# Performance work log

Hardware: AMD Instinct MI355X
Metric: run time of the kernel (lower is better)

The kernel has to match this reference:

```python
import jax, jax.numpy as jnp
import numpy as np

DIM = 512
HEADS = 8
DIM_HEAD = 64
DIM_INNER = HEADS * DIM_HEAD  # 512
SCALE = DIM_HEAD ** -0.5


def setup_inputs() -> dict:
    key = jax.random.key(0)
    k1, k2, k3 = jax.random.split(key, 3)
    x = jax.random.normal(k1, (8, 2048, DIM), dtype=jnp.float32)
    # Linear weights (no bias). Stored as [in, out] for x @ W.
    w_qkv = jax.random.normal(k2, (DIM, 3 * DIM_INNER), dtype=jnp.float32) * (DIM ** -0.5)
    w_out = jax.random.normal(k3, (DIM_INNER, DIM), dtype=jnp.float32) * (DIM_INNER ** -0.5)
    return {"x": x, "w_qkv": w_qkv, "w_out": w_out}


def reference(x, w_qkv, w_out):
    b, n, _ = x.shape
    qkv = x @ w_qkv  # [b, n, 3*h*d]
    qkv = qkv.reshape(b, n, 3, HEADS, DIM_HEAD)
    qkv = jnp.transpose(qkv, (2, 0, 3, 1, 4))  # [3, b, h, n, d]
    q, k, v = qkv[0], qkv[1], qkv[2]
    q = q * SCALE
    sim = jnp.einsum('bhid,bhjd->bhij', q, k)
    attn = jax.nn.softmax(sim, axis=-1)
    out = jnp.einsum('bhij,bhjd->bhid', attn, v)  # [b, h, n, d]
    out = jnp.transpose(out, (0, 2, 1, 3)).reshape(b, n, DIM_INNER)
    return out @ w_out
```

## Files before the change

kernel.cpp:

```cpp
#include <hip/hip_runtime.h>
#include <hip/hip_bf16.h>
#include <stdint.h>


#define NB 8
#define SEQ 2048
#define DIMM 512
#define HEADS 8
#define DHEAD 64
#define MTOT (NB * SEQ)

typedef __attribute__((ext_vector_type(8))) short bf16x8;
typedef __attribute__((ext_vector_type(4))) float f32x4;
typedef __attribute__((ext_vector_type(16))) float f32x16;
typedef __attribute__((ext_vector_type(4))) uint u32x4;

typedef __attribute__((address_space(1))) const void gconst_void;
typedef __attribute__((address_space(3))) void lds_void;

__device__ __forceinline__ ushort f2b(float f) {
  union { float f; uint32_t u; } c; c.f = f;
  return (ushort)((c.u + 0x7FFFu + ((c.u >> 16) & 1u)) >> 16);
}

__device__ __forceinline__ uint cvtpk(float lo, float hi) {
  uint r;
  asm("v_cvt_pk_bf16_f32 %0, %1, %2" : "=v"(r) : "v"(lo), "v"(hi));
  return r;
}
__device__ __forceinline__ void plswap(uint& a, uint& b) {
  asm("v_permlane32_swap_b32 %0, %1" : "+v"(a), "+v"(b));
}
__device__ __forceinline__ bf16x8 mk8(uint a, uint b, uint c, uint d) {
  u32x4 t = {a, b, c, d};
  return __builtin_bit_cast(bf16x8, t);
}

__global__ void cvt_bf16(const float* __restrict__ src, ushort* __restrict__ dst, int n8) {
  int i = blockIdx.x * blockDim.x + threadIdx.x;
  if (i >= n8) return;
  const float4* s = (const float4*)src;
  float4 a = s[2 * i], b = s[2 * i + 1];
  ushort o[8] = {f2b(a.x), f2b(a.y), f2b(a.z), f2b(a.w),
                 f2b(b.x), f2b(b.y), f2b(b.z), f2b(b.w)};
  *(uint4*)(dst + 8 * i) = *(const uint4*)o;
}

__global__ void cvt_transpose(const float* __restrict__ src, ushort* __restrict__ dst,
                              int R, int C) {
  __shared__ ushort tile[64][72];
  int nbc = C >> 6;
  int bc = blockIdx.x % nbc, br = blockIdx.x / nbc;
  int c0 = bc * 64, r0 = br * 64;
  #pragma unroll
  for (int p = 0; p < 16; ++p) {
    int e = p * 256 + threadIdx.x;
    int r = e >> 6, c = e & 63;
    tile[r][c] = f2b(src[(size_t)(r0 + r) * C + c0 + c]);
  }
  __syncthreads();
  #pragma unroll
  for (int p = 0; p < 16; ++p) {
    int e = p * 256 + threadIdx.x;
    int ct = e >> 6, rt = e & 63;
    dst[(size_t)(c0 + ct) * R + r0 + rt] = tile[rt][ct];
  }
}

__global__ __launch_bounds__(256) void gemm_qkv(
    const ushort* __restrict__ A, const ushort* __restrict__ Bt,
    ushort* __restrict__ qo, ushort* __restrict__ ko, ushort* __restrict__ vto) {
  __shared__ ushort As[128 * 64];
  __shared__ ushort Bs[128 * 64];
  const int tid = threadIdx.x;
  const int bid = blockIdx.x;
  const int sbid = (bid & 7) * 192 + (bid >> 3);
  const int bn = sbid % 12, bm = sbid / 12;
  const int wid = tid >> 6, lane = tid & 63;
  const int wm = (wid >> 1) * 64, wn = (wid & 1) * 64;
  const int lr = lane & 15, lk = (lane >> 4) * 8;
  const int fx = lr & 7;

  f32x4 acc[4][4] = {};
  const ushort* Ab = A + (size_t)(bm * 128) * DIMM;
  const ushort* Bb = Bt + (size_t)(bn * 128) * DIMM;

  const int srow = lane >> 3;
  const int sco = ((lane & 7) ^ srow) << 3;

  for (int kt = 0; kt < DIMM; kt += 64) {
    __syncthreads();
    #pragma unroll
    for (int j = 0; j < 4; ++j) {
      const int c = wid * 4 + j;
      const size_t ro = (size_t)(8 * c + srow) * DIMM + kt + sco;
      __builtin_amdgcn_global_load_lds((gconst_void*)(Ab + ro),
                                       (lds_void*)&As[c * 512], 16, 0, 0);
      __builtin_amdgcn_global_load_lds((gconst_void*)(Bb + ro),
                                       (lds_void*)&Bs[c * 512], 16, 0, 0);
    }
    asm volatile("s_waitcnt vmcnt(0)" ::: "memory");
    __syncthreads();

    #pragma unroll
    for (int kk = 0; kk < 64; kk += 32) {
      const int sb = (kk >> 3) + (lane >> 4);
      const int so = (sb ^ fx) << 3;
      bf16x8 af[4], bfr[4];
      #pragma unroll
      for (int i = 0; i < 4; ++i) af[i] = *(const bf16x8*)&As[(wm + i * 16 + lr) * 64 + so];
      #pragma unroll
      for (int j = 0; j < 4; ++j) bfr[j] = *(const bf16x8*)&Bs[(wn + j * 16 + lr) * 64 + so];
      #pragma unroll
      for (int i = 0; i < 4; ++i)
        #pragma unroll
        for (int j = 0; j < 4; ++j)
          acc[i][j] = __builtin_amdgcn_mfma_f32_16x16x32_bf16(af[i], bfr[j], acc[i][j], 0, 0, 0);
    }
  }

  const int rb = bm * 128 + wm + ((lane >> 4) << 2);
  const int cb = bn * 128 + wn + lr;
  const float QSCALE = 0.125f * 1.44269504f;
  #pragma unroll
  for (int i = 0; i < 4; ++i) {
    #pragma unroll
    for (int j = 0; j < 4; ++j) {
      int col = cb + j * 16;
      int t = col >> 9, h = (col >> 6) & 7, d = col & 63;
      f32x4 v = acc[i][j];
      #pragma unroll
      for (int e = 0; e < 4; ++e) {
        int row = rb + i * 16 + e;
        int b = row >> 11, n = row & 2047;
        float val = v[e];
        if (t == 0) {
          qo[(((size_t)b * HEADS + h) * SEQ + n) * DHEAD + d] = f2b(val * QSCALE);
        } else if (t == 1) {
          ko[(((size_t)b * HEADS + h) * SEQ + n) * DHEAD + d] = f2b(val);
        } else {
          vto[(((size_t)b * HEADS + h) * DHEAD + d) * SEQ + n] = f2b(val);
        }
      }
    }
  }
}

__global__ __launch_bounds__(256) void gemm_out(
    const ushort* __restrict__ A, const ushort* __restrict__ Bt, float* __restrict__ out) {
  __shared__ ushort As[128 * 64];
  __shared__ ushort Bs[128 * 64];
  const int tid = threadIdx.x;
  const int bid = blockIdx.x;
  const int sbid = (bid & 7) * 64 + (bid >> 3);
  const int bn = sbid % 4, bm = sbid / 4;
  const int wid = tid >> 6, lane = tid & 63;
  const int wm = (wid >> 1) * 64, wn = (wid & 1) * 64;
  const int lr = lane & 15, lk = (lane >> 4) * 8;
  const int fx = lr & 7;

  f32x4 acc[4][4] = {};
  const ushort* Ab = A + (size_t)(bm * 128) * DIMM;
  const ushort* Bb = Bt + (size_t)(bn * 128) * DIMM;

  const int srow = lane >> 3;
  const int sco = ((lane & 7) ^ srow) << 3;

  for (int kt = 0; kt < DIMM; kt += 64) {
    __syncthreads();
    #pragma unroll
    for (int j = 0; j < 4; ++j) {
      const int c = wid * 4 + j;
      const size_t ro = (size_t)(8 * c + srow) * DIMM + kt + sco;
      __builtin_amdgcn_global_load_lds((gconst_void*)(Ab + ro),
                                       (lds_void*)&As[c * 512], 16, 0, 0);
      __builtin_amdgcn_global_load_lds((gconst_void*)(Bb + ro),
                                       (lds_void*)&Bs[c * 512], 16, 0, 0);
    }
    asm volatile("s_waitcnt vmcnt(0)" ::: "memory");
    __syncthreads();

    #pragma unroll
    for (int kk = 0; kk < 64; kk += 32) {
      const int sb = (kk >> 3) + (lane >> 4);
      const int so = (sb ^ fx) << 3;
      bf16x8 af[4], bfr[4];
      #pragma unroll
      for (int i = 0; i < 4; ++i) af[i] = *(const bf16x8*)&As[(wm + i * 16 + lr) * 64 + so];
      #pragma unroll
      for (int j = 0; j < 4; ++j) bfr[j] = *(const bf16x8*)&Bs[(wn + j * 16 + lr) * 64 + so];
      #pragma unroll
      for (int i = 0; i < 4; ++i)
        #pragma unroll
        for (int j = 0; j < 4; ++j)
          acc[i][j] = __builtin_amdgcn_mfma_f32_16x16x32_bf16(af[i], bfr[j], acc[i][j], 0, 0, 0);
    }
  }

  const int rb = bm * 128 + wm + ((lane >> 4) << 2);
  const int cb = bn * 128 + wn + lr;
  #pragma unroll
  for (int i = 0; i < 4; ++i)
    #pragma unroll
    for (int j = 0; j < 4; ++j) {
      f32x4 v = acc[i][j];
      #pragma unroll
      for (int e = 0; e < 4; ++e)
        out[(size_t)(rb + i * 16 + e) * DIMM + cb + j * 16] = v[e];
    }
}

__global__ __launch_bounds__(256) void attn(
    const ushort* __restrict__ q, const ushort* __restrict__ k,
    const ushort* __restrict__ vt, ushort* __restrict__ ao) {
  __shared__ ushort Ks[64 * 64];
  __shared__ ushort Vs[64 * 64];

  const int tid = threadIdx.x;
  const int wid = tid >> 6, l = tid & 63;
  const int l31 = l & 31, hi = l >> 5;
  const int bh = blockIdx.x >> 4, qb = blockIdx.x & 15;
  const ushort* kb = k + (size_t)bh * SEQ * DHEAD;
  const ushort* vb = vt + (size_t)bh * DHEAD * SEQ;
  const int nq = qb * 128 + wid * 32 + l31;

  bf16x8 qf[4];
  const ushort* qrow = q + (size_t)bh * SEQ * DHEAD + (size_t)nq * DHEAD;
  #pragma unroll
  for (int ks = 0; ks < 4; ++ks)
    qf[ks] = *(const bf16x8*)(qrow + ks * 16 + hi * 8);

  f32x16 accO0 = {}, accO1 = {};
  float lrun = 0.f;

  const int sr = tid >> 3, sc = tid & 7;
  const int swz = (sc ^ (sr & 7)) << 3;
  uint4 k0 = *(const uint4*)(kb + (size_t)sr * DHEAD + sc * 8);
  uint4 k1 = *(const uint4*)(kb + (size_t)(sr + 32) * DHEAD + sc * 8);
  uint4 v0 = *(const uint4*)(vb + (size_t)sr * SEQ + sc * 8);
  uint4 v1 = *(const uint4*)(vb + (size_t)(sr + 32) * SEQ + sc * 8);

  const int fsx = (l31 & 7);

  for (int t = 0; t < SEQ / 64; ++t) {
    __syncthreads();
    *(uint4*)&Ks[sr * 64 + swz] = k0;
    *(uint4*)&Ks[(sr + 32) * 64 + swz] = k1;
    *(uint4*)&Vs[sr * 64 + swz] = v0;
    *(uint4*)&Vs[(sr + 32) * 64 + swz] = v1;
    __syncthreads();

    if (t + 1 < SEQ / 64) {
      int nt = (t + 1) * 64;
      k0 = *(const uint4*)(kb + (size_t)(nt + sr) * DHEAD + sc * 8);
      k1 = *(const uint4*)(kb + (size_t)(nt + sr + 32) * DHEAD + sc * 8);
      v0 = *(const uint4*)(vb + (size_t)sr * SEQ + nt + sc * 8);
      v1 = *(const uint4*)(vb + (size_t)(sr + 32) * SEQ + nt + sc * 8);
    }

    f32x16 s0 = {}, s1 = {};
    #pragma unroll
    for (int ks = 0; ks < 4; ++ks) {
      int g = (ks << 1) | hi;
      int so = (g ^ fsx) << 3;
      bf16x8 kf0 = *(const bf16x8*)&Ks[l31 * 64 + so];
      bf16x8 kf1 = *(const bf16x8*)&Ks[(32 + l31) * 64 + so];
      s0 = __builtin_amdgcn_mfma_f32_32x32x16_bf16(kf0, qf[ks], s0, 0, 0, 0);
      s1 = __builtin_amdgcn_mfma_f32_32x32x16_bf16(kf1, qf[ks], s1, 0, 0, 0);
    }

    float rs = 0.f;
    #pragma unroll
    for (int i = 0; i < 16; ++i) {
      s0[i] = __builtin_amdgcn_exp2f(s0[i]); rs += s0[i];
      s1[i] = __builtin_amdgcn_exp2f(s1[i]); rs += s1[i];
    }
    rs += __shfl_xor(rs, 32);
    lrun += rs;

    bf16x8 pf0, pf1, pf2, pf3;
    {
      uint a0 = cvtpk(s0[0], s0[1]),  a1 = cvtpk(s0[2], s0[3]);
      uint b0 = cvtpk(s0[4], s0[5]),  b1 = cvtpk(s0[6], s0[7]);
      plswap(a0, b0); plswap(a1, b1);
      pf0 = mk8(a0, a1, b0, b1);
      a0 = cvtpk(s0[8], s0[9]);   a1 = cvtpk(s0[10], s0[11]);
      b0 = cvtpk(s0[12], s0[13]); b1 = cvtpk(s0[14], s0[15]);
      plswap(a0, b0); plswap(a1, b1);
      pf1 = mk8(a0, a1, b0, b1);
      a0 = cvtpk(s1[0], s1[1]);   a1 = cvtpk(s1[2], s1[3]);
      b0 = cvtpk(s1[4], s1[5]);   b1 = cvtpk(s1[6], s1[7]);
      plswap(a0, b0); plswap(a1, b1);
      pf2 = mk8(a0, a1, b0, b1);
      a0 = cvtpk(s1[8], s1[9]);   a1 = cvtpk(s1[10], s1[11]);
      b0 = cvtpk(s1[12], s1[13]); b1 = cvtpk(s1[14], s1[15]);
      plswap(a0, b0); plswap(a1, b1);
      pf3 = mk8(a0, a1, b0, b1);
    }

    #pragma unroll
    for (int kk = 0; kk < 4; ++kk) {
      int g = (kk << 1) | hi;
      int so = (g ^ fsx) << 3;
      bf16x8 vf0 = *(const bf16x8*)&Vs[l31 * 64 + so];
      bf16x8 vf1 = *(const bf16x8*)&Vs[(32 + l31) * 64 + so];
      bf16x8 pk = (kk == 0) ? pf0 : (kk == 1) ? pf1 : (kk == 2) ? pf2 : pf3;
      accO0 = __builtin_amdgcn_mfma_f32_32x32x16_bf16(vf0, pk, accO0, 0, 0, 0);
      accO1 = __builtin_amdgcn_mfma_f32_32x32x16_bf16(vf1, pk, accO1, 0, 0, 0);
    }
  }

  const int b = bh >> 3, h = bh & 7;
  const float rl = 1.0f / lrun;
  ushort* aop = ao + ((size_t)b * SEQ + nq) * DIMM + h * DHEAD;
  #pragma unroll
  for (int gq = 0; gq < 4; ++gq) {
    {
      int d0 = 8 * gq + 4 * hi;
      uint u0 = (uint)f2b(accO0[4 * gq + 0] * rl) | ((uint)f2b(accO0[4 * gq + 1] * rl) << 16);
      uint u1 = (uint)f2b(accO0[4 * gq + 2] * rl) | ((uint)f2b(accO0[4 * gq + 3] * rl) << 16);
      *(uint2*)(aop + d0) = make_uint2(u0, u1);
    }
    {
      int d0 = 32 + 8 * gq + 4 * hi;
      uint u0 = (uint)f2b(accO1[4 * gq + 0] * rl) | ((uint)f2b(accO1[4 * gq + 1] * rl) << 16);
      uint u1 = (uint)f2b(accO1[4 * gq + 2] * rl) | ((uint)f2b(accO1[4 * gq + 3] * rl) << 16);
      *(uint2*)(aop + d0) = make_uint2(u0, u1);
    }
  }
}

extern "C" void kernel_launch(void* const* d_in, const int* in_sizes, int n_in,
                              void* d_out, int out_size, void* d_ws, size_t ws_size,
                              hipStream_t stream) {
  const float* x = (const float*)d_in[0];
  const float* wqkv = (const float*)d_in[1];
  const float* wout = (const float*)d_in[2];
  float* out = (float*)d_out;

  char* ws = (char*)d_ws;
  const size_t SZ = (size_t)MTOT * DIMM * 2;
  ushort* xb    = (ushort*)(ws);
  ushort* qw    = (ushort*)(ws + SZ);
  ushort* kw    = (ushort*)(ws + 2 * SZ);
  ushort* vtw   = (ushort*)(ws + 3 * SZ);
  ushort* aow   = (ushort*)(ws + 4 * SZ);
  ushort* wqkvT = (ushort*)(ws + 5 * SZ);
  ushort* woutT = (ushort*)(ws + 5 * SZ + (size_t)1536 * 512 * 2);

  hipLaunchKernelGGL(cvt_bf16, dim3(4096), dim3(256), 0, stream, x, xb, MTOT * DIMM / 8);
  hipLaunchKernelGGL(cvt_transpose, dim3(192), dim3(256), 0, stream, wqkv, wqkvT, 512, 1536);
  hipLaunchKernelGGL(cvt_transpose, dim3(64), dim3(256), 0, stream, wout, woutT, 512, 512);
  hipLaunchKernelGGL(gemm_qkv, dim3(128 * 12), dim3(256), 0, stream, xb, wqkvT, qw, kw, vtw);
  hipLaunchKernelGGL(attn, dim3(64 * 16), dim3(256), 0, stream, qw, kw, vtw, aow);
  hipLaunchKernelGGL(gemm_out, dim3(128 * 4), dim3(256), 0, stream, aow, woutT, out);
}
```

Measured before the change: 196.5 us.

## Load K/V MFMA fragments directly from global memory, dropping LDS staging

The attention kernel no longer stages K and V tiles through shared memory with register prefetch and two barriers per iteration. Each wave now reads its MFMA operand fragments straight from global memory (relying on L1/L2 for reuse across the four waves), and the launch bounds ask for 4 blocks per CU. This removes the LDS writes, the barriers and the swizzle arithmetic, but exposes global-load latency in the inner loop with no explicit prefetch and repeats each K/V load across waves.

```diff
diff --git a/kernel.cpp b/kernel.cpp
--- a/kernel.cpp
+++ b/kernel.cpp
@@ -210,12 +210,9 @@
     }
 }
 
-__global__ __launch_bounds__(256) void attn(
+__global__ __launch_bounds__(256, 4) void attn(
     const ushort* __restrict__ q, const ushort* __restrict__ k,
     const ushort* __restrict__ vt, ushort* __restrict__ ao) {
-  __shared__ ushort Ks[64 * 64];
-  __shared__ ushort Vs[64 * 64];
-
   const int tid = threadIdx.x;
   const int wid = tid >> 6, l = tid & 63;
   const int l31 = l & 31, hi = l >> 5;
@@ -233,38 +230,17 @@
   f32x16 accO0 = {}, accO1 = {};
   float lrun = 0.f;
 
-  const int sr = tid >> 3, sc = tid & 7;
-  const int swz = (sc ^ (sr & 7)) << 3;
-  uint4 k0 = *(const uint4*)(kb + (size_t)sr * DHEAD + sc * 8);
-  uint4 k1 = *(const uint4*)(kb + (size_t)(sr + 32) * DHEAD + sc * 8);
-  uint4 v0 = *(const uint4*)(vb + (size_t)sr * SEQ + sc * 8);
-  uint4 v1 = *(const uint4*)(vb + (size_t)(sr + 32) * SEQ + sc * 8);
-
-  const int fsx = (l31 & 7);
+  const ushort* kp0 = kb + (size_t)l31 * DHEAD + hi * 8;
+  const ushort* kp1 = kp0 + 32 * DHEAD;
+  const ushort* vp0 = vb + (size_t)l31 * SEQ + hi * 8;
+  const ushort* vp1 = vp0 + (size_t)32 * SEQ;
 
   for (int t = 0; t < SEQ / 64; ++t) {
-    __syncthreads();
-    *(uint4*)&Ks[sr * 64 + swz] = k0;
-    *(uint4*)&Ks[(sr + 32) * 64 + swz] = k1;
-    *(uint4*)&Vs[sr * 64 + swz] = v0;
-    *(uint4*)&Vs[(sr + 32) * 64 + swz] = v1;
-    __syncthreads();
-
-    if (t + 1 < SEQ / 64) {
-      int nt = (t + 1) * 64;
-      k0 = *(const uint4*)(kb + (size_t)(nt + sr) * DHEAD + sc * 8);
-      k1 = *(const uint4*)(kb + (size_t)(nt + sr + 32) * DHEAD + sc * 8);
-      v0 = *(const uint4*)(vb + (size_t)sr * SEQ + nt + sc * 8);
-      v1 = *(const uint4*)(vb + (size_t)(sr + 32) * SEQ + nt + sc * 8);
-    }
-
     f32x16 s0 = {}, s1 = {};
     #pragma unroll
     for (int ks = 0; ks < 4; ++ks) {
-      int g = (ks << 1) | hi;
-      int so = (g ^ fsx) << 3;
-      bf16x8 kf0 = *(const bf16x8*)&Ks[l31 * 64 + so];
-      bf16x8 kf1 = *(const bf16x8*)&Ks[(32 + l31) * 64 + so];
+      bf16x8 kf0 = *(const bf16x8*)(kp0 + ks * 16);
+      bf16x8 kf1 = *(const bf16x8*)(kp1 + ks * 16);
       s0 = __builtin_amdgcn_mfma_f32_32x32x16_bf16(kf0, qf[ks], s0, 0, 0, 0);
       s1 = __builtin_amdgcn_mfma_f32_32x32x16_bf16(kf1, qf[ks], s1, 0, 0, 0);
     }
@@ -300,14 +276,15 @@
 
     #pragma unroll
     for (int kk = 0; kk < 4; ++kk) {
-      int g = (kk << 1) | hi;
-      int so = (g ^ fsx) << 3;
-      bf16x8 vf0 = *(const bf16x8*)&Vs[l31 * 64 + so];
-      bf16x8 vf1 = *(const bf16x8*)&Vs[(32 + l31) * 64 + so];
+      bf16x8 vf0 = *(const bf16x8*)(vp0 + kk * 16);
+      bf16x8 vf1 = *(const bf16x8*)(vp1 + kk * 16);
       bf16x8 pk = (kk == 0) ? pf0 : (kk == 1) ? pf1 : (kk == 2) ? pf2 : pf3;
       accO0 = __builtin_amdgcn_mfma_f32_32x32x16_bf16(vf0, pk, accO0, 0, 0, 0);
       accO1 = __builtin_amdgcn_mfma_f32_32x32x16_bf16(vf1, pk, accO1, 0, 0, 0);
     }
+
+    kp0 += 64 * DHEAD;  kp1 += 64 * DHEAD;
+    vp0 += 64;          vp1 += 64;
   }
 
   const int b = bh >> 3, h = bh & 7;
```

Result: slower. 341.5 us (+73.9%).
